# Optimization experiments

Hardware: AMD Instinct MI355X
Metric: run time of the kernel (lower is better)

The kernel has to match this reference:

```python
import jax, jax.numpy as jnp
import numpy as np

B, F, V, D, K = 16384, 39, 30000, 16, 20
EPS = 1e-5


def bn_eval(x, g, b):
    # inference-mode BatchNorm1d with running_mean=0, running_var=1
    return g * x / jnp.sqrt(1.0 + EPS) + b


def setup_inputs() -> dict:
    key = jax.random.key(0)
    ks = jax.random.split(key, 12)
    x = jax.random.randint(ks[0], (B, F), 0, V)
    emb_table = jax.random.normal(ks[1], (F * V, D), dtype=jnp.float32) * 0.05
    w_c = jax.random.normal(ks[2], (F, F * D), dtype=jnp.float32) * 0.05
    w0 = jax.random.normal(ks[3], (1024, F * D), dtype=jnp.float32) * 0.04
    w1 = jax.random.normal(ks[4], (512, 1024), dtype=jnp.float32) * 0.03
    w_out = jax.random.normal(ks[5], (1, 512), dtype=jnp.float32) * 0.04
    return {
        'x': x, 'emb_table': emb_table,
        'w_c': w_c, 'b_c': jnp.zeros((F,)), 'g_c': jnp.ones((F,)), 'be_c': jnp.zeros((F,)),
        'w0': w0, 'b0': jnp.zeros((1024,)), 'g0': jnp.ones((1024,)), 'be0': jnp.zeros((1024,)),
        'w1': w1, 'b1': jnp.zeros((512,)), 'g1': jnp.ones((512,)), 'be1': jnp.zeros((512,)),
        'w_out': w_out, 'b_out': jnp.zeros((1,)),
    }


def reference(x, emb_table, w_c, b_c, g_c, be_c, w0, b0, g0, be0,
              w1, b1, g1, be1, w_out, b_out):
    offsets = jnp.arange(F, dtype=x.dtype) * V          # per-field offsets
    idx = x + offsets[None, :]                          # [B, F]
    emb = emb_table[idx]                                # [B, F, D] gather

    # controller_mlp: flatten (batch, D, F) layout like torch transpose(1,2)
    flat = jnp.transpose(emb, (0, 2, 1)).reshape(B, F * D)
    h = jax.nn.relu(bn_eval(flat @ w_c.T + b_c, g_c, be_c))
    scores = jax.nn.softmax(h, axis=1)                  # [B, F]

    # kmax_pooling: top-k field indices, sorted ascending, gather weights
    _, kidx = jax.lax.top_k(scores, K)
    kidx = jnp.sort(kidx, axis=1)                       # [B, K]
    w = jnp.take_along_axis(scores, kidx, axis=1)       # [B, K]

    # forward_select: gather selected field embeddings, weight them
    sel = jnp.take_along_axis(emb, kidx[:, :, None], axis=1)  # [B, K, D]
    weighted = sel * w[:, :, None]

    # scatter back into full field slots (unselected fields are zero)
    full = jnp.zeros((B, F, D), weighted.dtype)
    bidx = jnp.arange(B)[:, None]
    full = full.at[bidx, kidx].set(weighted)            # [B, F, D]

    z = jnp.transpose(full, (0, 2, 1)).reshape(B, F * D)
    z = jax.nn.relu(bn_eval(z @ w0.T + b0, g0, be0))
    z = jax.nn.relu(bn_eval(z @ w1.T + b1, g1, be1))
    out = jax.nn.sigmoid(z @ w_out.T + b_out)           # [B, 1]
    return out.squeeze(-1)
```

## Files before the change

kernel.cpp:

```cpp
#include <hip/hip_runtime.h>
#include <math.h>

#define B_SZ 16384
#define F_N 39
#define V_N 30000
#define D_N 16
#define K_SEL 20
#define FD 624
#define KP0 640
#define NCP 48
#define N0 1024
#define N1 512
#define CBR 16
#define ALD 648

typedef unsigned short u16;
typedef __attribute__((ext_vector_type(8))) short bf16x8;
typedef __attribute__((ext_vector_type(8))) unsigned short u16x8;
typedef __attribute__((ext_vector_type(4))) float f32x4;
typedef __attribute__((ext_vector_type(4))) unsigned short u16x4;

__device__ __forceinline__ u16 f2bf(float v) {
    union { float f; unsigned u; } x; x.f = v;
    unsigned r = x.u + 0x7fff + ((x.u >> 16) & 1);
    return (u16)(r >> 16);
}
__device__ __forceinline__ float bf2f(u16 v) {
    union { unsigned u; float f; } x; x.u = ((unsigned)v) << 16;
    return x.f;
}

#define GLD16(gp, lp) __builtin_amdgcn_global_load_lds( \
    (const __attribute__((address_space(1))) unsigned int*)(gp), \
    (__attribute__((address_space(3))) unsigned int*)(lp), 16, 0, 0)

__global__ void convert_kernel(const float* __restrict__ src, u16* __restrict__ dst,
                               int n_el)
{
    int i = blockIdx.x * blockDim.x + threadIdx.x;
    if (i < n_el) dst[i] = f2bf(src[i]);
}

__global__ void prep_w0_kernel(const float* __restrict__ w0, u16* __restrict__ w0p)
{
    int i = blockIdx.x * blockDim.x + threadIdx.x;
    if (i >= N0 * KP0) return;
    int n = i / KP0, kk = i - n * KP0;
    float v = 0.f;
    if (kk < FD) {
        int f = kk >> 4, d = kk & 15;
        v = w0[n * FD + d * F_N + f];
    }
    w0p[i] = f2bf(v);
}

__global__ void prep_wc_kernel(const float* __restrict__ w_c, u16* __restrict__ wcb)
{
    int i = blockIdx.x * blockDim.x + threadIdx.x;
    if (i >= NCP * KP0) return;
    int n = i / KP0, kk = i - n * KP0;
    float v = 0.f;
    if (n < F_N && kk < FD) {
        int f = kk >> 4, d = kk & 15;
        v = w_c[n * FD + d * F_N + f];
    }
    wcb[i] = f2bf(v);
}

__global__ void pad_params_kernel(const float* __restrict__ b_c,
                                  const float* __restrict__ g_c,
                                  const float* __restrict__ be_c,
                                  float* __restrict__ bp, float* __restrict__ gp,
                                  float* __restrict__ bep)
{
    int n = threadIdx.x;
    bp[n]  = (n < F_N) ? b_c[n]  : 0.f;
    gp[n]  = (n < F_N) ? g_c[n]  : 0.f;
    bep[n] = (n < F_N) ? be_c[n] : 0.f;
}

__global__ __launch_bounds__(64) void fused_controller_kernel(
    const int* __restrict__ x, const float* __restrict__ emb_table,
    const u16* __restrict__ wcb, const float* __restrict__ bcp,
    const float* __restrict__ gcp, const float* __restrict__ becp,
    u16* __restrict__ zb)
{
    __shared__ __align__(16) u16 Al[CBR * ALD];
    __shared__ float vv[CBR][49];

    const int lane = threadIdx.x;
    const int b0   = blockIdx.x * CBR;
    const int row  = lane >> 2;
    const int fg   = lane & 3;

    #pragma unroll
    for (int it = 0; it < 10; ++it) {
        const int f = fg + 4 * it;
        if (f < F_N) {
            const int xi = x[(b0 + row) * F_N + f];
            const float4* src =
                (const float4*)(emb_table + (size_t)(xi + f * V_N) * D_N);
            float4 v0 = src[0], v1 = src[1], v2 = src[2], v3 = src[3];
            u16x8 o0 = { f2bf(v0.x), f2bf(v0.y), f2bf(v0.z), f2bf(v0.w),
                         f2bf(v1.x), f2bf(v1.y), f2bf(v1.z), f2bf(v1.w) };
            u16x8 o1 = { f2bf(v2.x), f2bf(v2.y), f2bf(v2.z), f2bf(v2.w),
                         f2bf(v3.x), f2bf(v3.y), f2bf(v3.z), f2bf(v3.w) };
            *(u16x8*)&Al[row * ALD + f * D_N]     = o0;
            *(u16x8*)&Al[row * ALD + f * D_N + 8] = o1;
        }
    }
    __syncthreads();

    const int m = lane & 15;
    const int q = lane >> 4;
    f32x4 acc0 = {}, acc1 = {}, acc2 = {};
    const u16* ap  = &Al[m * ALD + q * 8];
    const u16* bp0 = wcb + (size_t)(0  + m) * KP0 + q * 8;
    const u16* bp1 = wcb + (size_t)(16 + m) * KP0 + q * 8;
    const u16* bp2 = wcb + (size_t)(32 + m) * KP0 + q * 8;
    #pragma unroll 4
    for (int k0 = 0; k0 < KP0; k0 += 32) {
        bf16x8 af = *(const bf16x8*)ap;
        bf16x8 b0 = *(const bf16x8*)bp0;
        bf16x8 b1 = *(const bf16x8*)bp1;
        bf16x8 b2 = *(const bf16x8*)bp2;
        acc0 = __builtin_amdgcn_mfma_f32_16x16x32_bf16(af, b0, acc0, 0, 0, 0);
        acc1 = __builtin_amdgcn_mfma_f32_16x16x32_bf16(af, b1, acc1, 0, 0, 0);
        acc2 = __builtin_amdgcn_mfma_f32_16x16x32_bf16(af, b2, acc2, 0, 0, 0);
        ap += 32; bp0 += 32; bp1 += 32; bp2 += 32;
    }

    const float rs = rsqrtf(1.0f + 1e-5f);
    #pragma unroll
    for (int j = 0; j < 3; ++j) {
        const f32x4 a = (j == 0) ? acc0 : (j == 1) ? acc1 : acc2;
        const int n = j * 16 + m;
        const float gn = gcp[n] * rs;
        const float bn = becp[n];
        const float bi = bcp[n];
        #pragma unroll
        for (int r = 0; r < 4; ++r)
            vv[q * 4 + r][n] = fmaxf(fmaf(gn, a[r] + bi, bn), 0.f);
    }
    __syncthreads();

    float e[10];
    float mloc = -1e30f;
    #pragma unroll
    for (int it = 0; it < 10; ++it) {
        const int f = fg + 4 * it;
        if (f < F_N) { e[it] = vv[row][f]; mloc = fmaxf(mloc, e[it]); }
    }
    mloc = fmaxf(mloc, __shfl_xor(mloc, 1, 64));
    mloc = fmaxf(mloc, __shfl_xor(mloc, 2, 64));
    float sloc = 0.f;
    #pragma unroll
    for (int it = 0; it < 10; ++it) {
        const int f = fg + 4 * it;
        if (f < F_N) { e[it] = expf(e[it] - mloc); sloc += e[it]; }
    }
    sloc += __shfl_xor(sloc, 1, 64);
    sloc += __shfl_xor(sloc, 2, 64);
    const float inv = 1.f / sloc;
    #pragma unroll
    for (int it = 0; it < 10; ++it) {
        const int f = fg + 4 * it;
        if (f < F_N) vv[row][f] = e[it];
    }
    __syncthreads();

    int rank[10] = {};
    for (int gg = 0; gg < F_N; ++gg) {
        const float o = vv[row][gg];
        #pragma unroll
        for (int it = 0; it < 10; ++it) {
            const int f = fg + 4 * it;
            if (f < F_N)
                rank[it] += (o > e[it] || (o == e[it] && gg < f)) ? 1 : 0;
        }
    }

    #pragma unroll
    for (int it = 0; it < 10; ++it) {
        const int f = fg + 4 * it;
        u16* dst = zb + (size_t)(b0 + row) * KP0 + f * D_N;
        if (f < F_N) {
            const float w = (rank[it] < K_SEL) ? e[it] * inv : 0.f;
            u16x8 a0 = *(u16x8*)&Al[row * ALD + f * D_N];
            u16x8 a1 = *(u16x8*)&Al[row * ALD + f * D_N + 8];
            u16x8 o0, o1;
            #pragma unroll
            for (int k = 0; k < 8; ++k) {
                o0[k] = f2bf(bf2f(a0[k]) * w);
                o1[k] = f2bf(bf2f(a1[k]) * w);
            }
            *(u16x8*)dst = o0;
            *(u16x8*)(dst + 8) = o1;
        } else if (f == F_N) {
            u16x8 zz = {0, 0, 0, 0, 0, 0, 0, 0};
            *(u16x8*)dst = zz;
            *(u16x8*)(dst + 8) = zz;
        }
    }
}

template<int STORE_BF16>
__global__ __launch_bounds__(256) void gemm_mfma_bn_relu(
    const u16* __restrict__ A, const u16* __restrict__ W,
    const float* __restrict__ bias, const float* __restrict__ g,
    const float* __restrict__ be, void* __restrict__ Cout,
    int M, int N, int Kp)
{
    __shared__ __align__(16) u16 As[128 * 32];
    __shared__ __align__(16) u16 Bs[128 * 32];

    const int t    = threadIdx.x;
    const int wave = t >> 6;
    const int lane = t & 63;
    const int wm   = wave >> 1, wn = wave & 1;
    const int m0   = blockIdx.x * 128;
    const int n0   = blockIdx.y * 128;

    const int lr    = lane >> 2;
    const int swz_u = (lane & 3) ^ ((lane >> 3) & 3);
    const u16* gA0 = A + (size_t)(m0 + wave * 32 + lr) * Kp + swz_u * 8;
    const u16* gA1 = gA0 + 16 * (size_t)Kp;
    const u16* gB0 = W + (size_t)(n0 + wave * 32 + lr) * Kp + swz_u * 8;
    const u16* gB1 = gB0 + 16 * (size_t)Kp;
    u16* lA0 = &As[(wave * 32)      * 32];
    u16* lA1 = &As[(wave * 32 + 16) * 32];
    u16* lB0 = &Bs[(wave * 32)      * 32];
    u16* lB1 = &Bs[(wave * 32 + 16) * 32];

    const int q    = lane >> 4;
    const int lr16 = lane & 15;

    int aoff[4], boff[4];
    #pragma unroll
    for (int i = 0; i < 4; ++i) {
        int ra = wm * 64 + i * 16 + lr16;
        aoff[i] = ra * 32 + ((q ^ ((ra >> 1) & 3)) * 8);
        int rb = wn * 64 + i * 16 + lr16;
        boff[i] = rb * 32 + ((q ^ ((rb >> 1) & 3)) * 8);
    }

    f32x4 acc[4][4] = {};

    for (int k0 = 0; k0 < Kp; k0 += 32) {
        GLD16(gA0, lA0); GLD16(gA1, lA1);
        GLD16(gB0, lB0); GLD16(gB1, lB1);
        gA0 += 32; gA1 += 32; gB0 += 32; gB1 += 32;
        __syncthreads();

        bf16x8 af[4], bfr[4];
        #pragma unroll
        for (int i = 0; i < 4; ++i) af[i]  = *(const bf16x8*)&As[aoff[i]];
        #pragma unroll
        for (int j = 0; j < 4; ++j) bfr[j] = *(const bf16x8*)&Bs[boff[j]];

        #pragma unroll
        for (int i = 0; i < 4; ++i)
            #pragma unroll
            for (int j = 0; j < 4; ++j)
                acc[i][j] = __builtin_amdgcn_mfma_f32_16x16x32_bf16(
                    af[i], bfr[j], acc[i][j], 0, 0, 0);
        __syncthreads();
    }

    const float rs = rsqrtf(1.0f + 1e-5f);
    #pragma unroll
    for (int j = 0; j < 4; ++j) {
        const int n = n0 + wn * 64 + j * 16 + lr16;
        const float bn_g = g[n] * rs;
        const float bn_b = be[n];
        const float bi   = bias[n];
        #pragma unroll
        for (int i = 0; i < 4; ++i) {
            const int mbase = m0 + wm * 64 + i * 16 + q * 4;
            #pragma unroll
            for (int r = 0; r < 4; ++r) {
                float v = acc[i][j][r] + bi;
                v = fmaxf(fmaf(bn_g, v, bn_b), 0.f);
                const size_t off = (size_t)(mbase + r) * N + n;
                if (STORE_BF16) ((u16*)Cout)[off] = f2bf(v);
                else            ((float*)Cout)[off] = v;
            }
        }
    }
}

__global__ __launch_bounds__(256) void out_kernel(
    const u16* __restrict__ h1b, const float* __restrict__ w_out,
    const float* __restrict__ b_out, float* __restrict__ out)
{
    const int wave = threadIdx.x >> 6;
    const int lane = threadIdx.x & 63;
    const int b = blockIdx.x * 4 + wave;
    const u16* row = h1b + (size_t)b * N1;
    float s = 0.f;
    #pragma unroll
    for (int i = 0; i < 8; ++i) {
        int k = lane + i * 64;
        s = fmaf(bf2f(row[k]), w_out[k], s);
    }
    #pragma unroll
    for (int off = 32; off; off >>= 1) s += __shfl_down(s, off, 64);
    if (lane == 0) out[b] = 1.f / (1.f + expf(-(s + b_out[0])));
}

extern "C" void kernel_launch(void* const* d_in, const int* in_sizes, int n_in,
                              void* d_out, int out_size, void* d_ws, size_t ws_size,
                              hipStream_t stream)
{
    const int*   x     = (const int*)  d_in[0];
    const float* emb   = (const float*)d_in[1];
    const float* w_c   = (const float*)d_in[2];
    const float* b_c   = (const float*)d_in[3];
    const float* g_c   = (const float*)d_in[4];
    const float* be_c  = (const float*)d_in[5];
    const float* w0    = (const float*)d_in[6];
    const float* b0    = (const float*)d_in[7];
    const float* g0    = (const float*)d_in[8];
    const float* be0   = (const float*)d_in[9];
    const float* w1    = (const float*)d_in[10];
    const float* b1    = (const float*)d_in[11];
    const float* g1    = (const float*)d_in[12];
    const float* be1   = (const float*)d_in[13];
    const float* w_out = (const float*)d_in[14];
    const float* b_out = (const float*)d_in[15];
    float* out = (float*)d_out;

    u16*   zb    = (u16*)d_ws;
    u16*   w0b   = zb    + (size_t)B_SZ * KP0;
    u16*   h0b   = w0b   + (size_t)N0 * KP0;
    u16*   w1b   = h0b   + (size_t)B_SZ * N0;
    u16*   h1b   = w1b   + (size_t)N1 * N0;
    u16*   wcb   = h1b   + (size_t)B_SZ * N1;
    float* bcp   = (float*)(wcb + (size_t)NCP * KP0);
    float* gcp   = bcp + NCP;
    float* becp  = gcp + NCP;

    pad_params_kernel<<<1, NCP, 0, stream>>>(b_c, g_c, be_c, bcp, gcp, becp);
    prep_wc_kernel<<<(NCP * KP0 + 255) / 256, 256, 0, stream>>>(w_c, wcb);
    prep_w0_kernel<<<(N0 * KP0 + 255) / 256, 256, 0, stream>>>(w0, w0b);
    convert_kernel<<<(N1 * N0 + 255) / 256, 256, 0, stream>>>(w1, w1b, N1 * N0);

    fused_controller_kernel<<<B_SZ / CBR, 64, 0, stream>>>(
        x, emb, wcb, bcp, gcp, becp, zb);

    gemm_mfma_bn_relu<1><<<dim3(B_SZ / 128, N0 / 128), 256, 0, stream>>>(
        zb, w0b, b0, g0, be0, h0b, B_SZ, N0, KP0);
    gemm_mfma_bn_relu<1><<<dim3(B_SZ / 128, N1 / 128), 256, 0, stream>>>(
        h0b, w1b, b1, g1, be1, h1b, B_SZ, N1, N0);

    out_kernel<<<B_SZ / 4, 256, 0, stream>>>(h1b, w_out, b_out, out);
}
```

Measured before the change: 243.9 us.

## Split controller K-loop across four waves and vectorize GEMM epilogue stores

The fused controller kernel grows from one wave to four. The embedding gather is spread over all 256 threads, and each wave takes a quarter of the K dimension, with partial accumulators reduced through shared memory. Softmax and top-k stay on wave 0, and the output write-back is spread over all threads. Separately, the GEMM swaps the MFMA operand order so each lane holds four consecutive columns, which allows vectorized bias/BN loads and 4-wide bf16 stores in place of scalar strided stores. The cost is extra shared memory and barriers, plus wave 0 doing serial softmax/rank work while the other waves sit idle.

After: 245.9 us. Within noise of the previous version (+0.8%).

```diff
diff --git a/kernel.cpp b/kernel.cpp
--- a/kernel.cpp
+++ b/kernel.cpp
@@ -79,7 +79,7 @@
     bep[n] = (n < F_N) ? be_c[n] : 0.f;
 }
 
-__global__ __launch_bounds__(64) void fused_controller_kernel(
+__global__ __launch_bounds__(256) void fused_controller_kernel(
     const int* __restrict__ x, const float* __restrict__ emb_table,
     const u16* __restrict__ wcb, const float* __restrict__ bcp,
     const float* __restrict__ gcp, const float* __restrict__ becp,
@@ -87,120 +87,134 @@
 {
     __shared__ __align__(16) u16 Al[CBR * ALD];
     __shared__ float vv[CBR][49];
-
-    const int lane = threadIdx.x;
+    __shared__ f32x4 part[4][64][3];
+    __shared__ float selw[CBR][F_N];
+
+    const int t    = threadIdx.x;
+    const int wave = t >> 6;
+    const int lane = t & 63;
     const int b0   = blockIdx.x * CBR;
-    const int row  = lane >> 2;
-    const int fg   = lane & 3;
-
-    #pragma unroll
-    for (int it = 0; it < 10; ++it) {
-        const int f = fg + 4 * it;
-        if (f < F_N) {
-            const int xi = x[(b0 + row) * F_N + f];
-            const float4* src =
-                (const float4*)(emb_table + (size_t)(xi + f * V_N) * D_N);
-            float4 v0 = src[0], v1 = src[1], v2 = src[2], v3 = src[3];
-            u16x8 o0 = { f2bf(v0.x), f2bf(v0.y), f2bf(v0.z), f2bf(v0.w),
-                         f2bf(v1.x), f2bf(v1.y), f2bf(v1.z), f2bf(v1.w) };
-            u16x8 o1 = { f2bf(v2.x), f2bf(v2.y), f2bf(v2.z), f2bf(v2.w),
-                         f2bf(v3.x), f2bf(v3.y), f2bf(v3.z), f2bf(v3.w) };
-            *(u16x8*)&Al[row * ALD + f * D_N]     = o0;
-            *(u16x8*)&Al[row * ALD + f * D_N + 8] = o1;
-        }
+
+    for (int p = t; p < CBR * F_N; p += 256) {
+        const int row = p / F_N;
+        const int f   = p - row * F_N;
+        const int xi  = x[b0 * F_N + p];
+        const float4* src = (const float4*)(emb_table + (size_t)(xi + f * V_N) * D_N);
+        float4 v0 = src[0], v1 = src[1], v2 = src[2], v3 = src[3];
+        u16x8 o0 = { f2bf(v0.x), f2bf(v0.y), f2bf(v0.z), f2bf(v0.w),
+                     f2bf(v1.x), f2bf(v1.y), f2bf(v1.z), f2bf(v1.w) };
+        u16x8 o1 = { f2bf(v2.x), f2bf(v2.y), f2bf(v2.z), f2bf(v2.w),
+                     f2bf(v3.x), f2bf(v3.y), f2bf(v3.z), f2bf(v3.w) };
+        *(u16x8*)&Al[row * ALD + f * D_N]     = o0;
+        *(u16x8*)&Al[row * ALD + f * D_N + 8] = o1;
     }
     __syncthreads();
 
     const int m = lane & 15;
     const int q = lane >> 4;
     f32x4 acc0 = {}, acc1 = {}, acc2 = {};
-    const u16* ap  = &Al[m * ALD + q * 8];
-    const u16* bp0 = wcb + (size_t)(0  + m) * KP0 + q * 8;
-    const u16* bp1 = wcb + (size_t)(16 + m) * KP0 + q * 8;
-    const u16* bp2 = wcb + (size_t)(32 + m) * KP0 + q * 8;
-    #pragma unroll 4
-    for (int k0 = 0; k0 < KP0; k0 += 32) {
-        bf16x8 af = *(const bf16x8*)ap;
-        bf16x8 b0 = *(const bf16x8*)bp0;
-        bf16x8 b1 = *(const bf16x8*)bp1;
-        bf16x8 b2 = *(const bf16x8*)bp2;
-        acc0 = __builtin_amdgcn_mfma_f32_16x16x32_bf16(af, b0, acc0, 0, 0, 0);
-        acc1 = __builtin_amdgcn_mfma_f32_16x16x32_bf16(af, b1, acc1, 0, 0, 0);
-        acc2 = __builtin_amdgcn_mfma_f32_16x16x32_bf16(af, b2, acc2, 0, 0, 0);
-        ap += 32; bp0 += 32; bp1 += 32; bp2 += 32;
-    }
-
-    const float rs = rsqrtf(1.0f + 1e-5f);
-    #pragma unroll
-    for (int j = 0; j < 3; ++j) {
-        const f32x4 a = (j == 0) ? acc0 : (j == 1) ? acc1 : acc2;
-        const int n = j * 16 + m;
-        const float gn = gcp[n] * rs;
-        const float bn = becp[n];
-        const float bi = bcp[n];
-        #pragma unroll
-        for (int r = 0; r < 4; ++r)
-            vv[q * 4 + r][n] = fmaxf(fmaf(gn, a[r] + bi, bn), 0.f);
-    }
+    {
+        const u16* ap  = &Al[m * ALD + wave * 160 + q * 8];
+        const u16* bp0 = wcb + (size_t)(0  + m) * KP0 + wave * 160 + q * 8;
+        const u16* bp1 = wcb + (size_t)(16 + m) * KP0 + wave * 160 + q * 8;
+        const u16* bp2 = wcb + (size_t)(32 + m) * KP0 + wave * 160 + q * 8;
+        #pragma unroll
+        for (int k = 0; k < 5; ++k) {
+            bf16x8 af = *(const bf16x8*)ap;
+            bf16x8 b0 = *(const bf16x8*)bp0;
+            bf16x8 b1 = *(const bf16x8*)bp1;
+            bf16x8 b2 = *(const bf16x8*)bp2;
+            acc0 = __builtin_amdgcn_mfma_f32_16x16x32_bf16(af, b0, acc0, 0, 0, 0);
+            acc1 = __builtin_amdgcn_mfma_f32_16x16x32_bf16(af, b1, acc1, 0, 0, 0);
+            acc2 = __builtin_amdgcn_mfma_f32_16x16x32_bf16(af, b2, acc2, 0, 0, 0);
+            ap += 32; bp0 += 32; bp1 += 32; bp2 += 32;
+        }
+    }
+    part[wave][lane][0] = acc0;
+    part[wave][lane][1] = acc1;
+    part[wave][lane][2] = acc2;
     __syncthreads();
 
-    float e[10];
-    float mloc = -1e30f;
-    #pragma unroll
-    for (int it = 0; it < 10; ++it) {
-        const int f = fg + 4 * it;
-        if (f < F_N) { e[it] = vv[row][f]; mloc = fmaxf(mloc, e[it]); }
-    }
-    mloc = fmaxf(mloc, __shfl_xor(mloc, 1, 64));
-    mloc = fmaxf(mloc, __shfl_xor(mloc, 2, 64));
-    float sloc = 0.f;
-    #pragma unroll
-    for (int it = 0; it < 10; ++it) {
-        const int f = fg + 4 * it;
-        if (f < F_N) { e[it] = expf(e[it] - mloc); sloc += e[it]; }
-    }
-    sloc += __shfl_xor(sloc, 1, 64);
-    sloc += __shfl_xor(sloc, 2, 64);
-    const float inv = 1.f / sloc;
-    #pragma unroll
-    for (int it = 0; it < 10; ++it) {
-        const int f = fg + 4 * it;
-        if (f < F_N) vv[row][f] = e[it];
-    }
-    __syncthreads();
-
-    int rank[10] = {};
-    for (int gg = 0; gg < F_N; ++gg) {
-        const float o = vv[row][gg];
+    if (wave == 0) {
+        f32x4 r0 = part[0][lane][0] + part[1][lane][0] + part[2][lane][0] + part[3][lane][0];
+        f32x4 r1 = part[0][lane][1] + part[1][lane][1] + part[2][lane][1] + part[3][lane][1];
+        f32x4 r2 = part[0][lane][2] + part[1][lane][2] + part[2][lane][2] + part[3][lane][2];
+
+        const float rs = rsqrtf(1.0f + 1e-5f);
+        #pragma unroll
+        for (int j = 0; j < 3; ++j) {
+            const f32x4 a = (j == 0) ? r0 : (j == 1) ? r1 : r2;
+            const int n = j * 16 + m;
+            const float gn = gcp[n] * rs;
+            const float bn = becp[n];
+            const float bi = bcp[n];
+            #pragma unroll
+            for (int r = 0; r < 4; ++r)
+                vv[q * 4 + r][n] = fmaxf(fmaf(gn, a[r] + bi, bn), 0.f);
+        }
+
+        const int row = lane >> 2;
+        const int fg  = lane & 3;
+        float e[10];
+        float mloc = -1e30f;
+        #pragma unroll
+        for (int it = 0; it < 10; ++it) {
+            const int f = fg + 4 * it;
+            if (f < F_N) { e[it] = vv[row][f]; mloc = fmaxf(mloc, e[it]); }
+        }
+        mloc = fmaxf(mloc, __shfl_xor(mloc, 1, 64));
+        mloc = fmaxf(mloc, __shfl_xor(mloc, 2, 64));
+        float sloc = 0.f;
+        #pragma unroll
+        for (int it = 0; it < 10; ++it) {
+            const int f = fg + 4 * it;
+            if (f < F_N) { e[it] = expf(e[it] - mloc); sloc += e[it]; }
+        }
+        sloc += __shfl_xor(sloc, 1, 64);
+        sloc += __shfl_xor(sloc, 2, 64);
+        const float inv = 1.f / sloc;
+        #pragma unroll
+        for (int it = 0; it < 10; ++it) {
+            const int f = fg + 4 * it;
+            if (f < F_N) vv[row][f] = e[it];
+        }
+
+        int rank[10] = {};
+        for (int gg = 0; gg < F_N; ++gg) {
+            const float o = vv[row][gg];
+            #pragma unroll
+            for (int it = 0; it < 10; ++it) {
+                const int f = fg + 4 * it;
+                if (f < F_N)
+                    rank[it] += (o > e[it] || (o == e[it] && gg < f)) ? 1 : 0;
+            }
+        }
         #pragma unroll
         for (int it = 0; it < 10; ++it) {
             const int f = fg + 4 * it;
             if (f < F_N)
-                rank[it] += (o > e[it] || (o == e[it] && gg < f)) ? 1 : 0;
-        }
-    }
-
-    #pragma unroll
-    for (int it = 0; it < 10; ++it) {
-        const int f = fg + 4 * it;
-        u16* dst = zb + (size_t)(b0 + row) * KP0 + f * D_N;
-        if (f < F_N) {
-            const float w = (rank[it] < K_SEL) ? e[it] * inv : 0.f;
-            u16x8 a0 = *(u16x8*)&Al[row * ALD + f * D_N];
-            u16x8 a1 = *(u16x8*)&Al[row * ALD + f * D_N + 8];
-            u16x8 o0, o1;
+                selw[row][f] = (rank[it] < K_SEL) ? e[it] * inv : 0.f;
+        }
+    }
+    __syncthreads();
+
+    for (int gp = t; gp < CBR * 40; gp += 256) {
+        const int row  = gp & 15;
+        const int slot = gp >> 4;
+        u16* dst = zb + (size_t)(b0 + row) * KP0 + slot * D_N;
+        u16x8 o0 = {0,0,0,0,0,0,0,0}, o1 = {0,0,0,0,0,0,0,0};
+        if (slot < F_N) {
+            const float w = selw[row][slot];
+            u16x8 a0 = *(u16x8*)&Al[row * ALD + slot * D_N];
+            u16x8 a1 = *(u16x8*)&Al[row * ALD + slot * D_N + 8];
             #pragma unroll
             for (int k = 0; k < 8; ++k) {
                 o0[k] = f2bf(bf2f(a0[k]) * w);
                 o1[k] = f2bf(bf2f(a1[k]) * w);
             }
-            *(u16x8*)dst = o0;
-            *(u16x8*)(dst + 8) = o1;
-        } else if (f == F_N) {
-            u16x8 zz = {0, 0, 0, 0, 0, 0, 0, 0};
-            *(u16x8*)dst = zz;
-            *(u16x8*)(dst + 8) = zz;
-        }
+        }
+        *(u16x8*)dst = o0;
+        *(u16x8*)(dst + 8) = o1;
     }
 }
 
@@ -263,28 +277,33 @@
             #pragma unroll
             for (int j = 0; j < 4; ++j)
                 acc[i][j] = __builtin_amdgcn_mfma_f32_16x16x32_bf16(
-                    af[i], bfr[j], acc[i][j], 0, 0, 0);
+                    bfr[j], af[i], acc[i][j], 0, 0, 0);
         __syncthreads();
     }
 
     const float rs = rsqrtf(1.0f + 1e-5f);
     #pragma unroll
     for (int j = 0; j < 4; ++j) {
-        const int n = n0 + wn * 64 + j * 16 + lr16;
-        const float bn_g = g[n] * rs;
-        const float bn_b = be[n];
-        const float bi   = bias[n];
+        const int nb = n0 + wn * 64 + j * 16 + q * 4;
+        const float4 bi4 = *(const float4*)&bias[nb];
+        const float4 g4  = *(const float4*)&g[nb];
+        const float4 be4 = *(const float4*)&be[nb];
         #pragma unroll
         for (int i = 0; i < 4; ++i) {
-            const int mbase = m0 + wm * 64 + i * 16 + q * 4;
+            const int m = m0 + wm * 64 + i * 16 + lr16;
+            u16x4 ob;
+            float4 of;
             #pragma unroll
             for (int r = 0; r < 4; ++r) {
-                float v = acc[i][j][r] + bi;
-                v = fmaxf(fmaf(bn_g, v, bn_b), 0.f);
-                const size_t off = (size_t)(mbase + r) * N + n;
-                if (STORE_BF16) ((u16*)Cout)[off] = f2bf(v);
-                else            ((float*)Cout)[off] = v;
+                float v = acc[i][j][r] + (&bi4.x)[r];
+                v = fmaxf(fmaf((&g4.x)[r] * rs, v, (&be4.x)[r]), 0.f);
+                if (STORE_BF16) ob[r] = f2bf(v);
+                else            (&of.x)[r] = v;
             }
+            if (STORE_BF16)
+                *(u16x4*)((u16*)Cout + (size_t)m * N + nb) = ob;
+            else
+                *(float4*)((float*)Cout + (size_t)m * N + nb) = of;
         }
     }
 }
@@ -345,7 +364,7 @@
     prep_w0_kernel<<<(N0 * KP0 + 255) / 256, 256, 0, stream>>>(w0, w0b);
     convert_kernel<<<(N1 * N0 + 255) / 256, 256, 0, stream>>>(w1, w1b, N1 * N0);
 
-    fused_controller_kernel<<<B_SZ / CBR, 64, 0, stream>>>(
+    fused_controller_kernel<<<B_SZ / CBR, 256, 0, stream>>>(
         x, emb, wcb, bcp, gcp, becp, zb);
 
     gemm_mfma_bn_relu<1><<<dim3(B_SZ / 128, N0 / 128), 256, 0, stream>>>(
```
